# Kernel optimization log

Measured on AMD Instinct MI355X. Metric: run time of the kernel, lower is better.

## Reference

```python
import jax, jax.numpy as jnp
import numpy as np

ALPHA = 0.6
LOSS_WEIGHT = 1.0
BIG = 1e9


def _centered_meshgrid(M):
    # centered per-cell coordinates within an MxM block, (row, col) order
    c = jnp.arange(M, dtype=jnp.float32) - (M - 1) / 2.0
    yy, xx = jnp.meshgrid(c, c, indexing='ij')
    return jnp.stack([yy, xx], axis=-1)  # [M, M, 2]


def setup_inputs() -> dict:
    key = jax.random.key(0)
    k1, k2, k3 = jax.random.split(key, 3)
    B, H, W, M, K = 4, 64, 64, 8, 64
    pred_scores = jax.random.normal(k1, (B, H * W, K), dtype=jnp.float32)
    pred_offsets = jax.random.normal(k2, (B, H * W, K, 2), dtype=jnp.float32) * 0.5
    target = jax.random.randint(k3, (B, H * M, W * M), 0, 2, dtype=jnp.int32)
    return {"pred_scores": pred_scores, "pred_offsets": pred_offsets,
            "target": target, "H": H, "W": W, "M": M}


def _forward(pred_scores, pred_offsets, target, H, W, M):
    B = target.shape[0]
    K = pred_scores.shape[-1]
    T = M * M
    HW = H * W

    tgt = (target > 0).astype(jnp.int32)
    # [B,H,M,W,M] -> [B,H,W,M,M] -> [B,HW,T]
    tgt = tgt.reshape(B, H, M, W, M).transpose(0, 1, 3, 2, 4).reshape(B, HW, T)

    # stable descending sort of targets (positives first)
    order = jnp.argsort(-tgt, axis=-1, stable=True)          # [B,HW,T]
    block_target = jnp.take_along_axis(tgt, order, axis=-1)  # [B,HW,T]

    base_off = _centered_meshgrid(M).reshape(T, 2) / M       # [T,2]
    mask_offsets = base_off[order]                           # [B,HW,T,2]

    # broadcast cost: [B,HW,K,T]
    loc_cost = jnp.abs(pred_offsets[:, :, :, None, :] - mask_offsets[:, :, None, :, :]).sum(-1)
    cls_cost = jnp.abs(jax.nn.sigmoid(pred_scores)[..., None]
                       - block_target[:, :, None, :].astype(pred_scores.dtype))
    cost = (loc_cost ** 0.8) * (cls_cost ** 0.2) * block_target[:, :, None, :].astype(pred_scores.dtype)
    cost = jax.lax.stop_gradient(cost)  # assignment is non-differentiable

    # batched greedy assignment: for each target (in sorted order) pick the
    # cheapest not-yet-assigned prediction slot
    cost_t = jnp.moveaxis(cost, -1, 0)               # [T,B,HW,K]
    assigned0 = jnp.zeros((B, HW, K), dtype=bool)
    kidx = jnp.arange(K)

    def step(assigned, c):
        c = jnp.where(assigned, BIG, c)
        idx = jnp.argmin(c, axis=-1)                 # [B,HW]
        assigned = assigned | (kidx[None, None, :] == idx[..., None])
        return assigned, idx

    _, assign = jax.lax.scan(step, assigned0, cost_t)
    assignment = jnp.moveaxis(assign, 0, -1)          # [B,HW,T] in [0,K)

    bi = jnp.arange(B)[:, None, None]
    ni = jnp.arange(HW)[None, :, None]
    target_scores = jnp.zeros((B, HW, K), jnp.int32).at[bi, ni, assignment].set(block_target)
    target_offsets = jnp.zeros_like(pred_offsets).at[bi, ni, assignment].set(
        mask_offsets.astype(pred_offsets.dtype))

    num_pos = jnp.maximum(jnp.count_nonzero(target_scores), 1).astype(pred_scores.dtype)
    # first-call EMA: old = initial = num_pos -> normalizer = num_pos
    normalizer = num_pos

    t = target_scores.astype(pred_scores.dtype)
    p = jax.nn.sigmoid(pred_scores)
    ce = -(t * jax.nn.log_sigmoid(pred_scores) + (1.0 - t) * jax.nn.log_sigmoid(-pred_scores))
    p_t = p * t + (1.0 - p) * (1.0 - t)
    focal = ce * (1.0 - p_t) ** 2 * (ALPHA * t + (1.0 - ALPHA) * (1.0 - t))
    obj_loss = focal.sum()

    loc_loss = (jnp.abs(pred_offsets - target_offsets).sum(-1) * t).sum()

    return LOSS_WEIGHT * (obj_loss / normalizer + 10.0 * loc_loss / normalizer)


def reference(pred_scores, pred_offsets, target, H, W, M):
    return _forward(pred_scores, pred_offsets, target, H, W, M)
```

## Files before the change

### kernel.cpp

```cpp
#include <hip/hip_runtime.h>
#include <math.h>

#define HW  4096
#define KK  64
#define BLK 256
#define BLOCKS_PER_WG 16

__device__ __forceinline__ unsigned umin32(unsigned a, unsigned b) { return a < b ? a : b; }

__device__ __forceinline__ float softplusf(float x) {
    return fmaxf(x, 0.0f) + log1pf(expf(-fabsf(x)));
}

__global__ __launch_bounds__(BLK) void assign_loss_kernel(
    const float4* __restrict__ ps4,
    const float4* __restrict__ po4,
    const int4*   __restrict__ tgt4,
    float* __restrict__ pobj,
    float* __restrict__ ploc,
    int*   __restrict__ pnp)
{
    const int lane = threadIdx.x & 63;
    const int wib  = threadIdx.x >> 6;
    const int wv   = blockIdx.x * 4 + wib;
    const int g    = lane >> 4;
    const int q    = lane & 15;
    const int bid  = wv * 4 + g;
    const int b    = bid >> 12;
    const int n    = bid & (HW - 1);
    const int h    = n >> 6, w = n & 63;

    const float4 sc = ps4[bid * 16 + q];
    const float4 pa = po4[bid * 32 + q * 2];
    const float4 pb = po4[bid * 32 + q * 2 + 1];
    const int4 tv = tgt4[(b * 512 + h * 8 + (q >> 1)) * 128 + w * 2 + (q & 1)];

    float p0[4] = {pa.x, pa.z, pb.x, pb.z};
    float p1[4] = {pa.y, pa.w, pb.y, pb.w};
    float s[4]  = {sc.x, sc.y, sc.z, sc.w};

    const int bbit[4] = {tv.x > 0, tv.y > 0, tv.z > 0, tv.w > 0};
    int cnt = bbit[0] + bbit[1] + bbit[2] + bbit[3];

    const unsigned long long BL0 = __ballot(bbit[0]);
    const unsigned long long BL1 = __ballot(bbit[1]);
    const unsigned long long BL2 = __ballot(bbit[2]);
    const unsigned long long BL3 = __ballot(bbit[3]);
    const int sh = g * 16;
    unsigned wm[4] = {
        (unsigned)(BL0 >> sh) & 0xFFFFu, (unsigned)(BL1 >> sh) & 0xFFFFu,
        (unsigned)(BL2 >> sh) & 0xFFFFu, (unsigned)(BL3 >> sh) & 0xFFFFu };

    float sig[4], cl[4], locl[4];
    #pragma unroll
    for (int u = 0; u < 4; ++u) {
        sig[u]  = 1.0f / (1.0f + expf(-s[u]));
        cl[u]   = sqrtf(sqrtf(1.0f - sig[u]));
        locl[u] = 0.0f;
    }

    const float FINF = __builtin_huge_valf();

    for (int qt = 0; qt < 16; ++qt) {
        const float by  = (float)(qt >> 1) * 0.125f - 0.4375f;
        const float bx0 = (qt & 1) ? 0.0625f : -0.4375f;
        #pragma unroll
        for (int v = 0; v < 4; ++v) {
            const float bxv = bx0 + 0.125f * (float)v;
            const unsigned live = wm[v] & 1u;
            float l[4]; unsigned k[4];
            #pragma unroll
            for (int u = 0; u < 4; ++u) {
                l[u] = fabsf(p0[u] - by) + fabsf(p1[u] - bxv);
                k[u] = (__float_as_uint(l[u] * cl[u]) & ~63u) | (unsigned)(q * 4 + u);
            }
            unsigned x = umin32(umin32(k[0], k[1]), umin32(k[2], k[3]));
            x = umin32(x, (unsigned)__builtin_amdgcn_ds_swizzle((int)x, 0x041F));
            x = umin32(x, (unsigned)__builtin_amdgcn_ds_swizzle((int)x, 0x081F));
            x = umin32(x, (unsigned)__builtin_amdgcn_ds_swizzle((int)x, 0x101F));
            x = umin32(x, (unsigned)__builtin_amdgcn_ds_swizzle((int)x, 0x201F));
            const unsigned adj = x | (live - 1u);
            #pragma unroll
            for (int u = 0; u < 4; ++u) {
                const bool win = (k[u] == adj);
                cl[u]   = win ? FINF : cl[u];
                locl[u] = win ? l[u] : locl[u];
            }
        }
        wm[0] >>= 1; wm[1] >>= 1; wm[2] >>= 1; wm[3] >>= 1;
    }

    float focal = 0.0f, locs = 0.0f;
    #pragma unroll
    for (int u = 0; u < 4; ++u) {
        const bool asg = (cl[u] > 1e30f);
        const float ce  = asg ? softplusf(-s[u]) : softplusf(s[u]);
        const float p_t = asg ? sig[u] : (1.0f - sig[u]);
        const float om  = 1.0f - p_t;
        focal += ce * om * om * (asg ? 0.6f : 0.4f);
        locs  += locl[u];
    }

    #pragma unroll
    for (int o = 32; o; o >>= 1) {
        focal += __shfl_xor(focal, o, 64);
        locs  += __shfl_xor(locs,  o, 64);
        cnt   += __shfl_xor(cnt,   o, 64);
    }

    __shared__ float sobj[4], sloc[4];
    __shared__ int   snp[4];
    if (lane == 0) { sobj[wib] = focal; sloc[wib] = locs; snp[wib] = cnt; }
    __syncthreads();
    if (threadIdx.x == 0) {
        float o = 0.0f, l = 0.0f; int np = 0;
        #pragma unroll
        for (int t = 0; t < 4; ++t) { o += sobj[t]; l += sloc[t]; np += snp[t]; }
        pobj[blockIdx.x] = o;
        ploc[blockIdx.x] = l;
        pnp [blockIdx.x] = np;
    }
}

__global__ __launch_bounds__(256) void finalize_kernel(
    const float* __restrict__ pobj,
    const float* __restrict__ ploc,
    const int*   __restrict__ pnp,
    int nb, float* __restrict__ out)
{
    __shared__ double so[256], sl[256];
    __shared__ long long sn[256];
    double o = 0.0, l = 0.0;
    long long np = 0;
    for (int i = threadIdx.x; i < nb; i += 256) {
        o  += (double)pobj[i];
        l  += (double)ploc[i];
        np += (long long)pnp[i];
    }
    so[threadIdx.x] = o; sl[threadIdx.x] = l; sn[threadIdx.x] = np;
    __syncthreads();
    for (int st = 128; st; st >>= 1) {
        if (threadIdx.x < st) {
            so[threadIdx.x] += so[threadIdx.x + st];
            sl[threadIdx.x] += sl[threadIdx.x + st];
            sn[threadIdx.x] += sn[threadIdx.x + st];
        }
        __syncthreads();
    }
    if (threadIdx.x == 0) {
        long long npos = sn[0] > 1 ? sn[0] : 1;
        out[0] = (float)((so[0] + 10.0 * sl[0]) / (double)npos);
    }
}

extern "C" void kernel_launch(void* const* d_in, const int* in_sizes, int n_in,
                              void* d_out, int out_size, void* d_ws, size_t ws_size,
                              hipStream_t stream) {
    const float4* ps4  = (const float4*)d_in[0];
    const float4* po4  = (const float4*)d_in[1];
    const int4*   tgt4 = (const int4*)d_in[2];

    const int total_blocks = in_sizes[0] / KK;
    const int nwg = total_blocks / BLOCKS_PER_WG;

    float* pobj = (float*)d_ws;
    float* ploc = pobj + nwg;
    int*   pnp  = (int*)(ploc + nwg);

    assign_loss_kernel<<<nwg, BLK, 0, stream>>>(ps4, po4, tgt4, pobj, ploc, pnp);
    finalize_kernel<<<1, 256, 0, stream>>>(pobj, ploc, pnp, nwg, (float*)d_out);
}
```

Before: 38.77 us.

## Iterate only over positive targets and use DPP row min reduction

The greedy assignment loop now walks only over the positive target cells, taken from bitmasks with ffs, instead of stepping through all 64 cells with a liveness mask. The target load is remapped so the bit order follows row-major cell index order. The 16-lane min reduction moves from ds_swizzle to inline-asm DPP row_ror v_min_u32, which avoids LDS-path latency. A per-slot dead mask replaces the infinity-cost marking. In exchange the loop becomes data-dependent, and the wave runs until its densest group finishes.

```diff
diff --git a/kernel.cpp b/kernel.cpp
--- a/kernel.cpp
+++ b/kernel.cpp
@@ -4,7 +4,7 @@
 #define HW  4096
 #define KK  64
 #define BLK 256
-#define BLOCKS_PER_WG 16
+#define BPW 4
 
 __device__ __forceinline__ unsigned umin32(unsigned a, unsigned b) { return a < b ? a : b; }
 
@@ -12,20 +12,32 @@
     return fmaxf(x, 0.0f) + log1pf(expf(-fabsf(x)));
 }
 
+__device__ __forceinline__ unsigned group_min_u32(unsigned x) {
+    asm("s_nop 1\n\t"
+        "v_min_u32_dpp %0, %0, %0 row_ror:1 row_mask:0xf bank_mask:0xf\n\t"
+        "s_nop 1\n\t"
+        "v_min_u32_dpp %0, %0, %0 row_ror:2 row_mask:0xf bank_mask:0xf\n\t"
+        "s_nop 1\n\t"
+        "v_min_u32_dpp %0, %0, %0 row_ror:4 row_mask:0xf bank_mask:0xf\n\t"
+        "s_nop 1\n\t"
+        "v_min_u32_dpp %0, %0, %0 row_ror:8 row_mask:0xf bank_mask:0xf\n\t"
+        "s_nop 1"
+        : "+v"(x));
+    return x;
+}
+
 __global__ __launch_bounds__(BLK) void assign_loss_kernel(
     const float4* __restrict__ ps4,
     const float4* __restrict__ po4,
-    const int4*   __restrict__ tgt4,
-    float* __restrict__ pobj,
-    float* __restrict__ ploc,
-    int*   __restrict__ pnp)
+    const int*    __restrict__ tgt,
+    float* __restrict__ pobj, float* __restrict__ ploc, int* __restrict__ pnp)
 {
     const int lane = threadIdx.x & 63;
     const int wib  = threadIdx.x >> 6;
     const int wv   = blockIdx.x * 4 + wib;
     const int g    = lane >> 4;
     const int q    = lane & 15;
-    const int bid  = wv * 4 + g;
+    const int bid  = wv * BPW + g;
     const int b    = bid >> 12;
     const int n    = bid & (HW - 1);
     const int h    = n >> 6, w = n & 63;
@@ -33,25 +45,30 @@
     const float4 sc = ps4[bid * 16 + q];
     const float4 pa = po4[bid * 32 + q * 2];
     const float4 pb = po4[bid * 32 + q * 2 + 1];
-    const int4 tv = tgt4[(b * 512 + h * 8 + (q >> 1)) * 128 + w * 2 + (q & 1)];
-
     float p0[4] = {pa.x, pa.z, pb.x, pb.z};
     float p1[4] = {pa.y, pa.w, pb.y, pb.w};
-    float s[4]  = {sc.x, sc.y, sc.z, sc.w};
+    float s [4] = {sc.x, sc.y, sc.z, sc.w};
 
-    const int bbit[4] = {tv.x > 0, tv.y > 0, tv.z > 0, tv.w > 0};
-    int cnt = bbit[0] + bbit[1] + bbit[2] + bbit[3];
+    const int rb = (b * 512 + h * 8 + (q >> 3)) * 512 + w * 8 + (q & 7);
+    int bb[4];
+    #pragma unroll
+    for (int v = 0; v < 4; ++v) bb[v] = tgt[rb + v * 1024] > 0;
+    int cnt = bb[0] + bb[1] + bb[2] + bb[3];
 
-    const unsigned long long BL0 = __ballot(bbit[0]);
-    const unsigned long long BL1 = __ballot(bbit[1]);
-    const unsigned long long BL2 = __ballot(bbit[2]);
-    const unsigned long long BL3 = __ballot(bbit[3]);
+    const unsigned long long B0 = __ballot(bb[0]);
+    const unsigned long long B1 = __ballot(bb[1]);
+    const unsigned long long B2 = __ballot(bb[2]);
+    const unsigned long long B3 = __ballot(bb[3]);
     const int sh = g * 16;
-    unsigned wm[4] = {
-        (unsigned)(BL0 >> sh) & 0xFFFFu, (unsigned)(BL1 >> sh) & 0xFFFFu,
-        (unsigned)(BL2 >> sh) & 0xFFFFu, (unsigned)(BL3 >> sh) & 0xFFFFu };
+    const unsigned w0 = (unsigned)(B0 >> sh) & 0xFFFFu;
+    const unsigned w1 = (unsigned)(B1 >> sh) & 0xFFFFu;
+    const unsigned w2 = (unsigned)(B2 >> sh) & 0xFFFFu;
+    const unsigned w3 = (unsigned)(B3 >> sh) & 0xFFFFu;
+    unsigned mlo = w0 | (w1 << 16);
+    unsigned mhi = w2 | (w3 << 16);
 
     float sig[4], cl[4], locl[4];
+    unsigned dead[4] = {0u, 0u, 0u, 0u};
     #pragma unroll
     for (int u = 0; u < 4; ++u) {
         sig[u]  = 1.0f / (1.0f + expf(-s[u]));
@@ -59,41 +76,37 @@
         locl[u] = 0.0f;
     }
 
-    const float FINF = __builtin_huge_valf();
+    while (__any((mlo | mhi) != 0u)) {
+        const unsigned gd = ((mlo | mhi) == 0u) ? ~0u : 0u;
+        const int t = (mlo != 0u) ? (__ffs(mlo) - 1) : (31 + __ffs(mhi));
+        const unsigned nhi = (mlo == 0u) ? (mhi & (mhi - 1u)) : mhi;
+        mlo &= (mlo - 1u);
+        mhi = nhi;
 
-    for (int qt = 0; qt < 16; ++qt) {
-        const float by  = (float)(qt >> 1) * 0.125f - 0.4375f;
-        const float bx0 = (qt & 1) ? 0.0625f : -0.4375f;
+        const float by = (float)(t >> 3) * 0.125f - 0.4375f;
+        const float bx = (float)(t & 7)  * 0.125f - 0.4375f;
+
+        float l[4]; unsigned kc[4];
         #pragma unroll
-        for (int v = 0; v < 4; ++v) {
-            const float bxv = bx0 + 0.125f * (float)v;
-            const unsigned live = wm[v] & 1u;
-            float l[4]; unsigned k[4];
-            #pragma unroll
-            for (int u = 0; u < 4; ++u) {
-                l[u] = fabsf(p0[u] - by) + fabsf(p1[u] - bxv);
-                k[u] = (__float_as_uint(l[u] * cl[u]) & ~63u) | (unsigned)(q * 4 + u);
-            }
-            unsigned x = umin32(umin32(k[0], k[1]), umin32(k[2], k[3]));
-            x = umin32(x, (unsigned)__builtin_amdgcn_ds_swizzle((int)x, 0x041F));
-            x = umin32(x, (unsigned)__builtin_amdgcn_ds_swizzle((int)x, 0x081F));
-            x = umin32(x, (unsigned)__builtin_amdgcn_ds_swizzle((int)x, 0x101F));
-            x = umin32(x, (unsigned)__builtin_amdgcn_ds_swizzle((int)x, 0x201F));
-            const unsigned adj = x | (live - 1u);
-            #pragma unroll
-            for (int u = 0; u < 4; ++u) {
-                const bool win = (k[u] == adj);
-                cl[u]   = win ? FINF : cl[u];
-                locl[u] = win ? l[u] : locl[u];
-            }
+        for (int u = 0; u < 4; ++u) {
+            l[u]  = fabsf(p0[u] - by) + fabsf(p1[u] - bx);
+            kc[u] = (__float_as_uint(l[u] * cl[u]) & ~63u) | (unsigned)(q * 4 + u);
         }
-        wm[0] >>= 1; wm[1] >>= 1; wm[2] >>= 1; wm[3] >>= 1;
+        unsigned x = umin32(umin32(kc[0] | dead[0], kc[1] | dead[1]),
+                            umin32(kc[2] | dead[2], kc[3] | dead[3])) | gd;
+        x = group_min_u32(x);
+        #pragma unroll
+        for (int u = 0; u < 4; ++u) {
+            const bool win = (kc[u] == x);
+            dead[u] = win ? ~0u : dead[u];
+            locl[u] = win ? l[u] : locl[u];
+        }
     }
 
     float focal = 0.0f, locs = 0.0f;
     #pragma unroll
     for (int u = 0; u < 4; ++u) {
-        const bool asg = (cl[u] > 1e30f);
+        const bool asg = (dead[u] != 0u);
         const float ce  = asg ? softplusf(-s[u]) : softplusf(s[u]);
         const float p_t = asg ? sig[u] : (1.0f - sig[u]);
         const float om  = 1.0f - p_t;
@@ -101,21 +114,22 @@
         locs  += locl[u];
     }
 
+    float fc = focal, lc = locs; int cc = cnt;
     #pragma unroll
     for (int o = 32; o; o >>= 1) {
-        focal += __shfl_xor(focal, o, 64);
-        locs  += __shfl_xor(locs,  o, 64);
-        cnt   += __shfl_xor(cnt,   o, 64);
+        fc += __shfl_xor(fc, o, 64);
+        lc += __shfl_xor(lc, o, 64);
+        cc += __shfl_xor(cc, o, 64);
     }
 
     __shared__ float sobj[4], sloc[4];
     __shared__ int   snp[4];
-    if (lane == 0) { sobj[wib] = focal; sloc[wib] = locs; snp[wib] = cnt; }
+    if (lane == 0) { sobj[wib] = fc; sloc[wib] = lc; snp[wib] = cc; }
     __syncthreads();
     if (threadIdx.x == 0) {
         float o = 0.0f, l = 0.0f; int np = 0;
         #pragma unroll
-        for (int t = 0; t < 4; ++t) { o += sobj[t]; l += sloc[t]; np += snp[t]; }
+        for (int u = 0; u < 4; ++u) { o += sobj[u]; l += sloc[u]; np += snp[u]; }
         pobj[blockIdx.x] = o;
         ploc[blockIdx.x] = l;
         pnp [blockIdx.x] = np;
@@ -156,17 +170,17 @@
 extern "C" void kernel_launch(void* const* d_in, const int* in_sizes, int n_in,
                               void* d_out, int out_size, void* d_ws, size_t ws_size,
                               hipStream_t stream) {
-    const float4* ps4  = (const float4*)d_in[0];
-    const float4* po4  = (const float4*)d_in[1];
-    const int4*   tgt4 = (const int4*)d_in[2];
+    const float4* ps4 = (const float4*)d_in[0];
+    const float4* po4 = (const float4*)d_in[1];
+    const int*    tgt = (const int*)d_in[2];
 
     const int total_blocks = in_sizes[0] / KK;
-    const int nwg = total_blocks / BLOCKS_PER_WG;
+    const int nwg = total_blocks / 16;
 
     float* pobj = (float*)d_ws;
     float* ploc = pobj + nwg;
     int*   pnp  = (int*)(ploc + nwg);
 
-    assign_loss_kernel<<<nwg, BLK, 0, stream>>>(ps4, po4, tgt4, pobj, ploc, pnp);
+    assign_loss_kernel<<<nwg, BLK, 0, stream>>>(ps4, po4, tgt, pobj, ploc, pnp);
     finalize_kernel<<<1, 256, 0, stream>>>(pobj, ploc, pnp, nwg, (float*)d_out);
 }
```

After: 34.38 us. -11.3%, faster.
